# Optimization experiments

Hardware: AMD Instinct MI355X
Metric: run time of the kernel (lower is better)

Reference implementation:

```python
import jax, jax.numpy as jnp
import numpy as np

B, T, V, CI = 1024, 256, 90, 128  # batch, in_channels(=frames), joints(hardcoded 90), inter_channels
EPS = 1e-5


def _bn(x, g, b, m, v):
    # BatchNorm1d in eval mode over channel dim of (B, C, V)
    return (x - m[None, :, None]) * (g * jax.lax.rsqrt(v + EPS))[None, :, None] + b[None, :, None]


def _conv1x1(x, w, b):
    # Conv1d kernel_size=1: (B, Cin, V) x (Cout, Cin) -> (B, Cout, V)
    return jnp.einsum('btv,ct->bcv', x, w) + b[None, :, None]


def setup_inputs() -> dict:
    key = jax.random.key(0)
    ks = iter(jax.random.split(key, 64))
    def nrm(shape, scale=1.0):
        return jax.random.normal(next(ks), shape, jnp.float32) * scale
    p = {}
    p['x1'] = nrm((B, T, V))
    p['x2'] = nrm((B, T, V))
    for nm in ('g', 'th', 'ph'):
        p[nm + '_bn_g'] = 1.0 + 0.1 * nrm((T,))
        p[nm + '_bn_b'] = 0.1 * nrm((T,))
        p[nm + '_bn_m'] = 0.1 * nrm((T,))
        p[nm + '_bn_v'] = jax.random.uniform(next(ks), (T,), jnp.float32, 0.5, 1.5)
        p[nm + '_w'] = nrm((CI, T), T ** -0.5)
        p[nm + '_b'] = 0.01 * nrm((CI,))
    p['W_w'] = nrm((T, CI), CI ** -0.5)
    p['W_b'] = 0.01 * nrm((T,))
    p['W_bn_g'] = 1.0 + 0.1 * nrm((T,))
    p['W_bn_b'] = 0.1 * nrm((T,))
    p['W_bn_m'] = 0.1 * nrm((T,))
    p['W_bn_v'] = jax.random.uniform(next(ks), (T,), jnp.float32, 0.5, 1.5)
    p['qt_w'] = nrm((CI, T), T ** -0.5); p['qt_b'] = 0.01 * nrm((CI,))
    p['ks_w'] = nrm((CI, V), V ** -0.5); p['ks_b'] = 0.01 * nrm((CI,))
    p['qs_w'] = nrm((CI, V), V ** -0.5); p['qs_b'] = 0.01 * nrm((CI,))
    p['kt_w'] = nrm((CI, T), T ** -0.5); p['kt_b'] = 0.01 * nrm((CI,))
    return p


def reference(x1, x2, g_bn_g, g_bn_b, g_bn_m, g_bn_v, g_w, g_b,
              th_bn_g, th_bn_b, th_bn_m, th_bn_v, th_w, th_b,
              ph_bn_g, ph_bn_b, ph_bn_m, ph_bn_v, ph_w, ph_b,
              W_w, W_b, W_bn_g, W_bn_b, W_bn_m, W_bn_v,
              qt_w, qt_b, ks_w, ks_b, qs_w, qs_b, kt_w, kt_b):
    # non-local branch projections (note: phi is applied to x2, theta only to x1)
    g_x1 = _conv1x1(_bn(x1, g_bn_g, g_bn_b, g_bn_m, g_bn_v), g_w, g_b)       # (B,CI,V)
    g_x2 = _conv1x1(_bn(x2, g_bn_g, g_bn_b, g_bn_m, g_bn_v), g_w, g_b)
    theta_x1 = _conv1x1(_bn(x1, th_bn_g, th_bn_b, th_bn_m, th_bn_v), th_w, th_b)
    phi_x1 = _conv1x1(_bn(x2, ph_bn_g, ph_bn_b, ph_bn_m, ph_bn_v), ph_w, ph_b)

    E_t = jnp.einsum('bcv,bdv->bcd', theta_x1, phi_x1)  # (B,CI,CI) = theta_x1 @ phi_x2^T
    E_s = jnp.einsum('bcv,bcw->bvw', theta_x1, phi_x1)  # (B,V,V)  = theta_x2 @ phi_x1
    attn_time_1 = jax.nn.softmax(E_t, axis=-1)
    attn_time_2 = jax.nn.softmax(E_t.transpose(0, 2, 1), axis=-1)
    attn_space_2 = jax.nn.softmax(E_s, axis=-1)            # softmax(energy_space_1)
    attn_space_1 = jax.nn.softmax(E_s.transpose(0, 2, 1), axis=-1)

    z1 = jnp.einsum('bcd,bdv,bvw->bcw', attn_time_2, g_x1, attn_space_2)  # (B,CI,V)
    z2 = jnp.einsum('bcd,bdv,bvw->bcw', attn_time_1, g_x2, attn_space_1)

    # cross interaction (1x1 attention: softmax over singleton dim -> 1, zero grad, kept for faithfulness)
    x1m_v = x1.mean(2)   # (B,T)
    x2m_t = x2.mean(1)   # (B,V)
    x1m_t = x1.mean(1)   # (B,V)
    x2m_v = x2.mean(2)   # (B,T)
    q_time = x1m_v @ qt_w.T + qt_b
    k_space = x2m_t @ ks_w.T + ks_b
    a_t2s = jax.nn.softmax(jnp.sum(q_time * k_space, -1, keepdims=True), axis=-1)[:, 0]  # (B,) == 1
    cross_t2s = a_t2s[:, None, None] * x1m_v[:, :, None]   # (B,T,1)
    q_space = x1m_t @ qs_w.T + qs_b
    k_time = x2m_v @ kt_w.T + kt_b
    a_s2t = jax.nn.softmax(jnp.sum(q_space * k_time, -1, keepdims=True), axis=-1)[:, 0]
    cross_s2t = a_s2t[:, None, None] * x2m_t[:, None, :]   # (B,1,V)

    # W: Conv1d(CI->T,1) then BatchNorm1d(T)
    proj1 = _bn(jnp.einsum('bcv,tc->btv', z1, W_w) + W_b[None, :, None], W_bn_g, W_bn_b, W_bn_m, W_bn_v)
    proj2 = _bn(jnp.einsum('bcv,tc->btv', z2, W_w) + W_b[None, :, None], W_bn_g, W_bn_b, W_bn_m, W_bn_v)

    w1 = jax.nn.softmax(jnp.stack([x1.mean((1, 2)), cross_s2t.mean((1, 2)), proj1.mean((1, 2))], axis=1), axis=1)
    fused_x1 = (w1[:, 0, None, None] * x1 + w1[:, 1, None, None] * cross_s2t
                + w1[:, 2, None, None] * proj1)
    w2 = jax.nn.softmax(jnp.stack([x2.mean((1, 2)), cross_t2s.mean((1, 2)), proj2.mean((1, 2))], axis=1), axis=1)
    fused_x2 = (w2[:, 0, None, None] * x2 + w2[:, 1, None, None] * cross_t2s
                + w2[:, 2, None, None] * proj2)
    return fused_x1, fused_x2
```

## Files before the change

### kernel.cpp

```cpp
#include <hip/hip_runtime.h>

typedef unsigned int u32;
typedef _Float16 f16;
typedef short s16;
typedef _Float16 f16x8 __attribute__((ext_vector_type(8)));
typedef short bf16x8 __attribute__((ext_vector_type(8)));
typedef float f32x4 __attribute__((ext_vector_type(4)));

#define MFMA16(a,b,c) __builtin_amdgcn_mfma_f32_16x16x32_f16(a,b,c,0,0,0)
#define MFMABF(a,b,c) __builtin_amdgcn_mfma_f32_16x16x32_bf16(a,b,c,0,0,0)

namespace {

constexpr int VV = 90, BTV = 256*90, NB = 1024, NT = 1024;

constexpr int XT  = 0;
constexpr int UT  = 0;
constexpr int OS1 = 0;
constexpr int US  = 17408;
constexpr int G1T = 26768;
constexpr int THT = 39824;
constexpr int PHT = 52880;
constexpr int X2  = 52880;
constexpr int G2T = 66448;
constexpr int M1o = 39824;
constexpr int M2o = 53136;
constexpr int Z1o = 26768;
constexpr int Z2o = 66448;
constexpr int OS2 = 39824;
constexpr int SBASE = 79504;
constexpr int oX1MV=0, oX2MT=256, oMRT=352, oISRT=480, oMCT=608, oISCT=736,
              oMRS=864, oISRS=960, oISCS=1056, oSCAL=1152, oMSP=1168;
constexpr int oRED1=608, oRED2=736;
constexpr int SWORDS = 1184;
constexpr int SMEM_BYTES = SBASE*2 + SWORDS*4;

constexpr size_t wThP=0, wGP=65536, wPhP=131072, wWP=196608,
  wBeTh=262144, wBeG=262656, wBePh=263168, wBwe=263680, wCsw=264704, wBwsum=265216;

__device__ __forceinline__ int swz(int row, int col){
  return col ^ (((row >> 3) & 3) << 4);
}

__device__ __forceinline__ f16x8 frag_ld(const f16* p, int stride){
  int l = threadIdx.x & 63;
  return *(const f16x8*)(p + (l & 15) * stride + (l >> 4) * 8);
}
__device__ __forceinline__ bf16x8 bfrag_ld(const s16* p, int stride){
  int l = threadIdx.x & 63;
  return *(const bf16x8*)(p + (l & 15) * stride + (l >> 4) * 8);
}
__device__ __forceinline__ f16x8 frag_ld_sw(const f16* p, int stride, int rowbase, int colbase){
  int l = threadIdx.x & 63;
  int row = rowbase + (l & 15);
  int col = (colbase + (l >> 4) * 8) ^ (((row >> 3) & 3) << 4);
  return *(const f16x8*)(p + row * stride + col);
}
__device__ __forceinline__ bf16x8 bfrag_ld_sw(const s16* p, int stride, int rowbase, int colbase){
  int l = threadIdx.x & 63;
  int row = rowbase + (l & 15);
  int col = (colbase + (l >> 4) * 8) ^ (((row >> 3) & 3) << 4);
  return *(const bf16x8*)(p + row * stride + col);
}
__device__ __forceinline__ s16 f2bf(float x){
  u32 u = __float_as_uint(x);
  u += 0x7FFFu + ((u >> 16) & 1u);
  return (s16)(u >> 16);
}
__device__ __forceinline__ float bf2f(s16 h){
  return __uint_as_float(((u32)(unsigned short)h) << 16);
}

__global__ void prep_weights(
    const float* __restrict__ th_w, const float* __restrict__ th_b,
    const float* __restrict__ th_bng, const float* __restrict__ th_bnb,
    const float* __restrict__ th_bnm, const float* __restrict__ th_bnv,
    const float* __restrict__ g_w, const float* __restrict__ g_b,
    const float* __restrict__ g_bng, const float* __restrict__ g_bnb,
    const float* __restrict__ g_bnm, const float* __restrict__ g_bnv,
    const float* __restrict__ ph_w, const float* __restrict__ ph_b,
    const float* __restrict__ ph_bng, const float* __restrict__ ph_bnb,
    const float* __restrict__ ph_bnm, const float* __restrict__ ph_bnv,
    const float* __restrict__ W_w, const float* __restrict__ W_b,
    const float* __restrict__ W_bng, const float* __restrict__ W_bnb,
    const float* __restrict__ W_bnm, const float* __restrict__ W_bnv,
    char* __restrict__ ws)
{
  __shared__ float red[256];
  const int b = blockIdx.x, tid = threadIdx.x;
  f16* ThP = (f16*)(ws + wThP); f16* GP = (f16*)(ws + wGP);
  f16* PhP = (f16*)(ws + wPhP); s16* WP = (s16*)(ws + wWP);
  float* beTh = (float*)(ws + wBeTh); float* beG = (float*)(ws + wBeG);
  float* bePh = (float*)(ws + wBePh); float* bwe = (float*)(ws + wBwe);
  float* csw = (float*)(ws + wCsw); float* bwsum = (float*)(ws + wBwsum);
  if (b < 128){
    const int c = b, t = tid;
    {
      float s = th_bng[t] * rsqrtf(th_bnv[t] + 1e-5f);
      float d = th_bnb[t] - th_bnm[t] * s;
      float w = th_w[c*256 + t];
      ThP[c*256 + t] = (f16)(w * s);
      red[tid] = w * d; __syncthreads();
      for (int o = 128; o > 0; o >>= 1){ if (tid < o) red[tid] += red[tid+o]; __syncthreads(); }
      if (tid == 0) beTh[c] = th_b[c] + red[0];
      __syncthreads();
    }
    {
      float s = g_bng[t] * rsqrtf(g_bnv[t] + 1e-5f);
      float d = g_bnb[t] - g_bnm[t] * s;
      float w = g_w[c*256 + t];
      GP[c*256 + t] = (f16)(w * s);
      red[tid] = w * d; __syncthreads();
      for (int o = 128; o > 0; o >>= 1){ if (tid < o) red[tid] += red[tid+o]; __syncthreads(); }
      if (tid == 0) beG[c] = g_b[c] + red[0];
      __syncthreads();
    }
    {
      float s = ph_bng[t] * rsqrtf(ph_bnv[t] + 1e-5f);
      float d = ph_bnb[t] - ph_bnm[t] * s;
      float w = ph_w[c*256 + t];
      PhP[c*256 + t] = (f16)(w * s);
      red[tid] = w * d; __syncthreads();
      for (int o = 128; o > 0; o >>= 1){ if (tid < o) red[tid] += red[tid+o]; __syncthreads(); }
      if (tid == 0) bePh[c] = ph_b[c] + red[0];
    }
  } else {
    const int t = (b - 128) * 2 + (tid >> 7);
    const int c = tid & 127;
    float sW = W_bng[t] * rsqrtf(W_bnv[t] + 1e-5f);
    WP[t*128 + c] = f2bf(W_w[t*128 + c] * sW);
    if (c == 0) bwe[t] = (W_b[t] - W_bnm[t]) * sW + W_bnb[t];
    {
      const int c2 = b - 128;
      float sT = W_bng[tid] * rsqrtf(W_bnv[tid] + 1e-5f);
      red[tid] = W_w[tid*128 + c2] * sT;
      __syncthreads();
      for (int o = 128; o > 0; o >>= 1){ if (tid < o) red[tid] += red[tid+o]; __syncthreads(); }
      if (tid == 0) csw[c2] = red[0];
      __syncthreads();
      if (b == 128){
        red[tid] = (W_b[tid] - W_bnm[tid]) * sT + W_bnb[tid];
        __syncthreads();
        for (int o = 128; o > 0; o >>= 1){ if (tid < o) red[tid] += red[tid+o]; __syncthreads(); }
        if (tid == 0) bwsum[0] = red[0];
      }
    }
  }
}

__global__ __launch_bounds__(NT, 1)
void stacif_main(const float* __restrict__ x1g, const float* __restrict__ x2g,
                 const char* __restrict__ ws, float* __restrict__ outg)
{
  extern __shared__ f16 sm[];
  float* Sf = (float*)(sm + SBASE);
  const int tid = threadIdx.x, bid = blockIdx.x;
  const int wid = tid >> 6, l = tid & 63;
  const float* __restrict__ x1b = x1g + (size_t)bid * BTV;
  const float* __restrict__ x2b = x2g + (size_t)bid * BTV;
  const f16* ThP = (const f16*)(ws + wThP);
  const f16* GP  = (const f16*)(ws + wGP);
  const f16* PhP = (const f16*)(ws + wPhP);
  const s16* WP  = (const s16*)(ws + wWP);
  const float* beTh = (const float*)(ws + wBeTh);
  const float* beG  = (const float*)(ws + wBeG);
  const float* bePh = (const float*)(ws + wBePh);
  const float* bwe  = (const float*)(ws + wBwe);
  const float* csw  = (const float*)(ws + wCsw);
  const float* bwsum = (const float*)(ws + wBwsum);
  s16* Up  = (s16*)(sm + UT);
  s16* USp = (s16*)(sm + US);

  const int tS = tid >> 2, qS = tid & 3, vB = qS * 23;

  {
    float r1[23];
    const float* p1 = x1b + tS * 90;
    #pragma unroll
    for (int j = 0; j < 23; ++j){
      int off = vB + j; off = (off < 90) ? off : 89;
      r1[j] = p1[off];
    }
    float a = 0.f;
    #pragma unroll
    for (int j = 0; j < 23; ++j) if (vB + j < 90) a += r1[j];
    a += __shfl_xor(a, 1); a += __shfl_xor(a, 2);
    if (qS == 0) Sf[oX1MV + tS] = a * (1.f/90.f);
    #pragma unroll
    for (int j = 0; j < 23; ++j){
      int v = vB + j;
      if (v < 90) sm[XT + v*272 + tS] = (f16)r1[j];
    }
  }
  {
    float r2[23];
    const float* p2 = x2b + tS * 90;
    #pragma unroll
    for (int j = 0; j < 23; ++j){
      int off = vB + j; off = (off < 90) ? off : 89;
      r2[j] = p2[off];
    }
    #pragma unroll
    for (int j = 0; j < 23; ++j){
      int v = vB + j;
      if (v < 90) sm[X2 + v*272 + tS] = (f16)r2[j];
    }
  }
  __syncthreads();

  {
    const int mat = wid >> 3;
    const int c0 = (wid & 7) * 16;
    const f16* Wm = mat ? GP : ThP;
    const float* beg = mat ? beG : beTh;
    f32x4 acc[6] = {};
    #pragma unroll
    for (int kk = 0; kk < 8; ++kk){
      f16x8 bfr = frag_ld(Wm + c0*256 + kk*32, 256);
      #pragma unroll
      for (int vt = 0; vt < 6; ++vt){
        f16x8 a = frag_ld(sm + XT + vt*16*272 + kk*32, 272);
        acc[vt] = MFMA16(a, bfr, acc[vt]);
      }
    }
    int c = c0 + (l & 15);
    float bias = beg[c];
    #pragma unroll
    for (int vt = 0; vt < 6; ++vt){
      #pragma unroll
      for (int r = 0; r < 4; ++r){
        int v = vt*16 + (l >> 4)*4 + r;
        float val = acc[vt][r] + bias;
        if (mat) ((s16*)(sm + G1T))[v*136 + c] = (v < VV) ? f2bf(val) : (s16)0;
        else     sm[THT + v*136 + swz(v, c)] = (v < VV) ? (f16)val : (f16)0.0f;
      }
    }
  }
  __syncthreads();

  if (tid < 768){
    int v = tid >> 3, p = tid & 7;
    float a = 0.f;
    for (int j = 0; j < 32; ++j) a += (float)sm[X2 + v*272 + p*32 + j];
    a += __shfl_xor(a, 1); a += __shfl_xor(a, 2); a += __shfl_xor(a, 4);
    if (p == 0 && v < VV) Sf[oX2MT + v] = a * (1.f/256.f);
  }
  {
    const int mat = wid >> 3;
    const int c0 = (wid & 7) * 16;
    const f16* Wm = mat ? GP : PhP;
    const float* beg = mat ? beG : bePh;
    f32x4 acc[6] = {};
    #pragma unroll
    for (int kk = 0; kk < 8; ++kk){
      f16x8 bfr = frag_ld(Wm + c0*256 + kk*32, 256);
      #pragma unroll
      for (int vt = 0; vt < 6; ++vt){
        f16x8 a = frag_ld(sm + X2 + vt*16*272 + kk*32, 272);
        acc[vt] = MFMA16(a, bfr, acc[vt]);
      }
    }
    __syncthreads();
    int c = c0 + (l & 15);
    float bias = beg[c];
    #pragma unroll
    for (int vt = 0; vt < 6; ++vt){
      #pragma unroll
      for (int r = 0; r < 4; ++r){
        int v = vt*16 + (l >> 4)*4 + r;
        float val = acc[vt][r] + bias;
        if (mat) ((s16*)(sm + G2T))[v*136 + c] = (v < VV) ? f2bf(val) : (s16)0;
        else     sm[PHT + v*136 + swz(v, c)] = (v < VV) ? (f16)val : (f16)0.0f;
      }
    }
  }
  __syncthreads();

  if (wid < 8){
    int c0 = wid * 16;
    int ca = c0 + (l & 15);
    f32x4 acc[8] = {};
    for (int kk = 0; kk < 3; ++kk){
      int vb = kk*32 + (l >> 4) * 8;
      int cas = swz(vb, ca);
      f16x8 a;
      #pragma unroll
      for (int bb = 0; bb < 8; ++bb) a[bb] = sm[THT + (vb + bb)*136 + cas];
      #pragma unroll
      for (int dt = 0; dt < 8; ++dt){
        int das = swz(vb, dt*16 + (l & 15));
        f16x8 bf;
        #pragma unroll
        for (int bb = 0; bb < 8; ++bb) bf[bb] = sm[PHT + (vb + bb)*136 + das];
        acc[dt] = MFMA16(a, bf, acc[dt]);
      }
    }
    #pragma unroll
    for (int dt = 0; dt < 8; ++dt){
      float m4 = fmaxf(fmaxf(acc[dt][0], acc[dt][1]), fmaxf(acc[dt][2], acc[dt][3]));
      m4 = fmaxf(m4, __shfl_xor(m4, 16));
      m4 = fmaxf(m4, __shfl_xor(m4, 32));
      if (l < 16) Up[(dt*16 + l)*136 + 128 + wid] = f2bf(m4);
    }
    #pragma unroll
    for (int r = 0; r < 4; ++r){
      float m = -3e38f;
      #pragma unroll
      for (int dt = 0; dt < 8; ++dt) m = fmaxf(m, acc[dt][r]);
      for (int sh = 1; sh < 16; sh <<= 1) m = fmaxf(m, __shfl_xor(m, sh));
      float s = 0.f;
      #pragma unroll
      for (int dt = 0; dt < 8; ++dt){ float e = __expf(acc[dt][r] - m); acc[dt][r] = e; s += e; }
      for (int sh = 1; sh < 16; sh <<= 1) s += __shfl_xor(s, sh);
      int row = c0 + (l >> 4)*4 + r;
      if ((l & 15) == 0){ Sf[oMRT + row] = m; Sf[oISRT + row] = 1.f / s; }
      #pragma unroll
      for (int dt = 0; dt < 8; ++dt) Up[row*136 + swz(row, dt*16 + (l & 15))] = f2bf(acc[dt][r]);
    }
  } else if (wid < 14){
    int v0 = (wid - 8) * 16;
    f32x4 acc[6] = {};
    for (int kk = 0; kk < 4; ++kk){
      f16x8 a = frag_ld_sw(sm + THT, 136, v0, kk*32);
      #pragma unroll
      for (int wt = 0; wt < 6; ++wt){
        f16x8 bfr = frag_ld_sw(sm + PHT, 136, wt*16, kk*32);
        acc[wt] = MFMA16(a, bfr, acc[wt]);
      }
    }
    float wmax = -3e38f;
    #pragma unroll
    for (int r = 0; r < 4; ++r){
      float m = 0.f;
      #pragma unroll
      for (int wt = 0; wt < 6; ++wt) m = fmaxf(m, acc[wt][r]);
      for (int sh = 1; sh < 16; sh <<= 1) m = fmaxf(m, __shfl_xor(m, sh));
      float s = 0.f;
      #pragma unroll
      for (int wt = 0; wt < 6; ++wt){
        float e = __expf(acc[wt][r] - m);
        bool valid = (wt*16 + (l & 15)) < VV;
        acc[wt][r] = valid ? e : 0.f;
        s += acc[wt][r];
      }
      for (int sh = 1; sh < 16; sh <<= 1) s += __shfl_xor(s, sh);
      int row = v0 + (l >> 4)*4 + r;
      if ((l & 15) == 0){ Sf[oMRS + row] = m; Sf[oISRS + row] = 1.f / s; }
      if (row < VV) wmax = fmaxf(wmax, m);
      if (row < VV){
        #pragma unroll
        for (int wt = 0; wt < 6; ++wt) USp[row*104 + wt*16 + (l & 15)] = f2bf(acc[wt][r]);
      }
    }
    wmax = fmaxf(wmax, __shfl_xor(wmax, 16));
    wmax = fmaxf(wmax, __shfl_xor(wmax, 32));
    if (l == 0) Sf[oMSP + (wid - 8)] = wmax;
  }
  __syncthreads();

  {
    int ch = wid >> 1;
    int c = (wid & 1) * 64 + l;
    bf16x8 pm8 = *(const bf16x8*)(Up + c*136 + 128);
    float mp = bf2f(pm8[0]);
    #pragma unroll
    for (int q = 1; q < 8; ++q) mp = fmaxf(mp, bf2f(pm8[q]));
    float s = 0.f;
    #pragma unroll
    for (int j = 0; j < 16; ++j){
      int d = ch*16 + j;
      float u = bf2f(Up[d*136 + swz(d, c)]);
      if (u > 0.f){
        float e1 = __expf(0.5f * (Sf[oMRT + d] - mp));
        s += (u * e1) * e1;
      }
    }
    float* PT = (float*)(sm + THT);
    PT[ch*128 + c] = s;
    if (ch == 0) PT[1024 + c] = mp;
  }
  if (tid < 768){
    int v = tid >> 3, p = tid & 7;
    float Ms = Sf[oMSP + 0];
    #pragma unroll
    for (int q = 1; q < 6; ++q) Ms = fmaxf(Ms, Sf[oMSP + q]);
    float s = 0.f;
    for (int j = 0; j < 12; ++j){
      int w = p*12 + j;
      if (w < VV){
        float u = bf2f(USp[w*104 + v]);
        if (u > 0.f) s += u * __expf(Sf[oMRS + w] - Ms);
      }
    }
    s += __shfl_xor(s, 1); s += __shfl_xor(s, 2); s += __shfl_xor(s, 4);
    if (p == 0) Sf[oISCS + v] = 1.f / fmaxf(s, 1e-30f);
  }
  if (tid == 0){
    float Ms = Sf[oMSP + 0];
    #pragma unroll
    for (int q = 1; q < 6; ++q) Ms = fmaxf(Ms, Sf[oMSP + q]);
    Sf[oSCAL + 8] = Ms;
  }
  __syncthreads();
  if (tid < 128){
    const float* PT = (const float*)(sm + THT);
    float s = 0.f;
    #pragma unroll
    for (int q = 0; q < 8; ++q) s += PT[q*128 + tid];
    Sf[oMCT + tid] = PT[1024 + tid];
    Sf[oISCT + tid] = 1.f / s;
  }
  __syncthreads();

  if (wid < 8){
    int c0 = wid * 16;
    const s16* G1 = (const s16*)(sm + G1T);
    s16* M1 = (s16*)(sm + M1o);
    int ca = c0 + (l & 15);
    float mctc = Sf[oMCT + ca];
    f32x4 acc[6] = {};
    #pragma unroll
    for (int kk = 0; kk < 4; ++kk){
      int db = kk*32 + (l >> 4) * 8;
      int cas = swz(db, ca);
      bf16x8 a;
      #pragma unroll
      for (int bb = 0; bb < 8; ++bb){
        float u = bf2f(Up[(db + bb)*136 + cas]);
        float val = 0.f;
        if (u > 0.f){
          float e1 = __expf(0.5f * (Sf[oMRT + db + bb] - mctc));
          val = (u * e1) * e1;
        }
        a[bb] = f2bf(val);
      }
      #pragma unroll
      for (int vt = 0; vt < 6; ++vt){
        bf16x8 bfv = bfrag_ld(G1 + vt*16*136 + kk*32, 136);
        acc[vt] = MFMABF(a, bfv, acc[vt]);
      }
    }
    #pragma unroll
    for (int vt = 0; vt < 6; ++vt){
      int v = vt*16 + (l & 15);
      float cs = (v < VV) ? Sf[oISRS + v] : 0.f;
      #pragma unroll
      for (int r = 0; r < 4; ++r){
        int c = c0 + (l >> 4)*4 + r;
        M1[c*104 + v] = f2bf(acc[vt][r] * Sf[oISCT + c] * cs);
      }
    }
  } else {
    int c0 = (wid - 8) * 16;
    const s16* G2 = (const s16*)(sm + G2T);
    s16* M2 = (s16*)(sm + M2o);
    f32x4 acc[6] = {};
    #pragma unroll
    for (int kk = 0; kk < 4; ++kk){
      bf16x8 a = bfrag_ld_sw(Up, 136, c0, kk*32);
      #pragma unroll
      for (int vt = 0; vt < 6; ++vt){
        bf16x8 bfv = bfrag_ld(G2 + vt*16*136 + kk*32, 136);
        acc[vt] = MFMABF(a, bfv, acc[vt]);
      }
    }
    #pragma unroll
    for (int vt = 0; vt < 6; ++vt){
      int v = vt*16 + (l & 15);
      float cs = (v < VV) ? Sf[oISCS + v] : 0.f;
      #pragma unroll
      for (int r = 0; r < 4; ++r){
        int c = c0 + (l >> 4)*4 + r;
        M2[c*104 + v] = f2bf(acc[vt][r] * Sf[oISRT + c] * cs);
      }
    }
  }
  __syncthreads();

  for (int pass = 0; pass < 3; ++pass){
    int u = wid + pass*16;
    bool isZ2 = u >= 24;
    int rem = isZ2 ? u - 24 : u;
    int w0 = (rem >> 2) * 16;
    int cq = rem & 3;
    int wa = w0 + (l & 15);
    const s16* Mx = (const s16*)(sm + (isZ2 ? M2o : M1o));
    s16* Z = (s16*)(sm + (isZ2 ? Z2o : Z1o));
    int wr = (wa < VV) ? wa : (VV - 1);
    float e_row = isZ2 ? __expf(Sf[oMRS + wr] - Sf[oSCAL + 8]) : 0.f;
    f32x4 acc[2] = {};
    #pragma unroll
    for (int kk = 0; kk < 3; ++kk){
      int vb = kk*32 + (l >> 4) * 8;
      bf16x8 a;
      if (!isZ2){
        #pragma unroll
        for (int bb = 0; bb < 8; ++bb){
          int v = vb + bb;
          a[bb] = (v < VV) ? USp[v*104 + wa] : (s16)0;
        }
      } else {
        bf16x8 uv = *(const bf16x8*)(USp + wr*104 + vb);
        #pragma unroll
        for (int bb = 0; bb < 8; ++bb){
          a[bb] = f2bf(bf2f(uv[bb]) * e_row);
        }
      }
      #pragma unroll
      for (int ct = 0; ct < 2; ++ct){
        bf16x8 bfv = bfrag_ld(Mx + (cq*2 + ct)*16*104 + kk*32, 104);
        acc[ct] = MFMABF(a, bfv, acc[ct]);
      }
    }
    #pragma unroll
    for (int ct = 0; ct < 2; ++ct){
      #pragma unroll
      for (int r = 0; r < 4; ++r){
        int row = w0 + (l >> 4)*4 + r;
        Z[row*136 + (cq*2 + ct)*16 + (l & 15)] = f2bf(acc[ct][r]);
      }
    }
  }
  __syncthreads();

  {
    int col = tid >> 3, zi = (tid >> 2) & 1, p = tid & 3;
    const s16* Z = (const s16*)(sm + (zi ? Z2o : Z1o));
    float s = 0.f;
    for (int j = 0; j < 23; ++j){
      int w = p*23 + j;
      if (w < VV) s += bf2f(Z[w*136 + col]);
    }
    s += __shfl_xor(s, 1); s += __shfl_xor(s, 2);
    if (p == 0){
      float* R = Sf + (zi ? oRED2 : oRED1);
      R[col] = csw[col] * s;
    }
  }
  __syncthreads();
  if (wid == 0){
    float s1 = Sf[oRED1 + l] + Sf[oRED1 + 64 + l];
    float s2 = Sf[oRED2 + l] + Sf[oRED2 + 64 + l];
    float t1 = Sf[oX1MV + l] + Sf[oX1MV + 64 + l] + Sf[oX1MV + 128 + l] + Sf[oX1MV + 192 + l];
    float t2 = (l < VV) ? Sf[oX2MT + l] : 0.f;
    if (l < 26) t2 += Sf[oX2MT + 64 + l];
    for (int sh = 1; sh < 64; sh <<= 1){
      s1 += __shfl_xor(s1, sh);
      s2 += __shfl_xor(s2, sh);
      t1 += __shfl_xor(t1, sh);
      t2 += __shfl_xor(t2, sh);
    }
    if (l == 0){
      float m1 = t1 * (1.f/256.f);
      float m2 = t2 * (1.f/90.f);
      float bws = bwsum[0];
      float mp1 = (s1 + 90.f*bws) * (1.f/23040.f);
      float mp2 = (s2 + 90.f*bws) * (1.f/23040.f);
      {
        float mx = fmaxf(m1, fmaxf(m2, mp1));
        float e0 = __expf(m1-mx), e1 = __expf(m2-mx), e2 = __expf(mp1-mx);
        float inv = 1.f/(e0+e1+e2);
        Sf[oSCAL+0] = e0*inv; Sf[oSCAL+1] = e1*inv; Sf[oSCAL+2] = e2*inv;
      }
      {
        float mx = fmaxf(m2, fmaxf(m1, mp2));
        float e0 = __expf(m2-mx), e1 = __expf(m1-mx), e2 = __expf(mp2-mx);
        float inv = 1.f/(e0+e1+e2);
        Sf[oSCAL+3] = e0*inv; Sf[oSCAL+4] = e1*inv; Sf[oSCAL+5] = e2*inv;
      }
    }
  }
  __syncthreads();

  for (int pass = 0; pass < 2; ++pass){
    int u = wid + pass*16;
    bool is2 = u & 1;
    int t0 = (u >> 1) * 16;
    const s16* Zp = (const s16*)(sm + (is2 ? Z2o : Z1o));
    f32x4 acc[6] = {};
    #pragma unroll
    for (int kk = 0; kk < 4; ++kk){
      bf16x8 a = bfrag_ld(WP + t0*128 + kk*32, 128);
      #pragma unroll
      for (int vt = 0; vt < 6; ++vt){
        bf16x8 bfr = bfrag_ld(Zp + vt*16*136 + kk*32, 136);
        acc[vt] = MFMABF(a, bfr, acc[vt]);
      }
    }
    f16* OS = sm + (is2 ? OS2 : OS1);
    float wb = is2 ? Sf[oSCAL+4] : Sf[oSCAL+1];
    float wc = is2 ? Sf[oSCAL+5] : Sf[oSCAL+2];
    #pragma unroll
    for (int r = 0; r < 4; ++r){
      int t = t0 + (l >> 4)*4 + r;
      float bw = bwe[t];
      float crossv = is2 ? Sf[oX1MV + t] : 0.f;
      #pragma unroll
      for (int vt = 0; vt < 6; ++vt){
        int v = vt*16 + (l & 15);
        if (v < VV){
          float cross = is2 ? crossv : Sf[oX2MT + v];
          OS[t*90 + v] = (f16)(wb * cross + wc * (acc[vt][r] + bw));
        }
      }
    }
  }
  __syncthreads();

  {
    float* out1 = outg + (size_t)bid * BTV;
    float* out2 = outg + (size_t)NB * BTV + (size_t)bid * BTV;
    const float4* x14 = (const float4*)x1b;
    const float4* x24 = (const float4*)x2b;
    float wa1 = Sf[oSCAL+0], wa2 = Sf[oSCAL+3];
    #pragma unroll
    for (int k = 0; k < 3; ++k){
      int e = (k*1024 + tid) * 8;
      if (e < BTV){
        float4 xa = x14[e/4], xb4 = x14[e/4 + 1];
        float4 xc = x24[e/4], xd4 = x24[e/4 + 1];
        f16x8 h1 = *(const f16x8*)(sm + OS1 + e);
        f16x8 h2 = *(const f16x8*)(sm + OS2 + e);
        float4 a1 = {wa1*xa.x + (float)h1[0], wa1*xa.y + (float)h1[1],
                     wa1*xa.z + (float)h1[2], wa1*xa.w + (float)h1[3]};
        float4 b1 = {wa1*xb4.x + (float)h1[4], wa1*xb4.y + (float)h1[5],
                     wa1*xb4.z + (float)h1[6], wa1*xb4.w + (float)h1[7]};
        float4 a2 = {wa2*xc.x + (float)h2[0], wa2*xc.y + (float)h2[1],
                     wa2*xc.z + (float)h2[2], wa2*xc.w + (float)h2[3]};
        float4 b2 = {wa2*xd4.x + (float)h2[4], wa2*xd4.y + (float)h2[5],
                     wa2*xd4.z + (float)h2[6], wa2*xd4.w + (float)h2[7]};
        *(float4*)(out1 + e)     = a1;
        *(float4*)(out1 + e + 4) = b1;
        *(float4*)(out2 + e)     = a2;
        *(float4*)(out2 + e + 4) = b2;
      }
    }
  }
}

}

extern "C" void kernel_launch(void* const* d_in, const int* in_sizes, int n_in,
                              void* d_out, int out_size, void* d_ws, size_t ws_size,
                              hipStream_t stream)
{
  (void)in_sizes; (void)n_in; (void)out_size; (void)ws_size;
  hipFuncSetAttribute((const void*)stacif_main,
                      hipFuncAttributeMaxDynamicSharedMemorySize, SMEM_BYTES);

  const float* x1 = (const float*)d_in[0];
  const float* x2 = (const float*)d_in[1];
  const float* g_bng = (const float*)d_in[2];
  const float* g_bnb = (const float*)d_in[3];
  const float* g_bnm = (const float*)d_in[4];
  const float* g_bnv = (const float*)d_in[5];
  const float* g_w   = (const float*)d_in[6];
  const float* g_b   = (const float*)d_in[7];
  const float* th_bng = (const float*)d_in[8];
  const float* th_bnb = (const float*)d_in[9];
  const float* th_bnm = (const float*)d_in[10];
  const float* th_bnv = (const float*)d_in[11];
  const float* th_w   = (const float*)d_in[12];
  const float* th_b   = (const float*)d_in[13];
  const float* ph_bng = (const float*)d_in[14];
  const float* ph_bnb = (const float*)d_in[15];
  const float* ph_bnm = (const float*)d_in[16];
  const float* ph_bnv = (const float*)d_in[17];
  const float* ph_w   = (const float*)d_in[18];
  const float* ph_b   = (const float*)d_in[19];
  const float* W_w    = (const float*)d_in[20];
  const float* W_b    = (const float*)d_in[21];
  const float* W_bng  = (const float*)d_in[22];
  const float* W_bnb  = (const float*)d_in[23];
  const float* W_bnm  = (const float*)d_in[24];
  const float* W_bnv  = (const float*)d_in[25];
  char* ws = (char*)d_ws;
  float* out = (float*)d_out;

  prep_weights<<<dim3(256), dim3(256), 0, stream>>>(
      th_w, th_b, th_bng, th_bnb, th_bnm, th_bnv,
      g_w, g_b, g_bng, g_bnb, g_bnm, g_bnv,
      ph_w, ph_b, ph_bng, ph_bnb, ph_bnm, ph_bnv,
      W_w, W_b, W_bng, W_bnb, W_bnm, W_bnv, ws);
  stacif_main<<<dim3(NB), dim3(NT), SMEM_BYTES, stream>>>(x1, x2, ws, out);
}
```

Before: 240.7 us.

## Store transposed theta/phi copies in LDS for vector MFMA fragment loads

The theta and phi projections are now written twice to shared memory: row-major without the XOR swizzle, and also transposed (channel-major, stride 104) into the region the x tile used before. The channel-attention GEMM then loads contiguous 8-wide fragments instead of gathering eight scalar f16 values per fragment, and the spatial GEMM drops its swizzled loads. Extra barriers are added so the transposed copies do not overwrite the input tile while it is still being read, and both GEMMs finish before their softmax writes. This trades extra LDS stores, possible bank conflicts from removing the swizzle, and an added barrier for much cheaper fragment loads.

```diff
diff --git a/kernel.cpp b/kernel.cpp
--- a/kernel.cpp
+++ b/kernel.cpp
@@ -15,6 +15,8 @@
 constexpr int VV = 90, BTV = 256*90, NB = 1024, NT = 1024;
 
 constexpr int XT  = 0;
+constexpr int TH2 = 0;
+constexpr int PH2 = 13312;
 constexpr int UT  = 0;
 constexpr int OS1 = 0;
 constexpr int US  = 17408;
@@ -49,12 +51,6 @@
 __device__ __forceinline__ bf16x8 bfrag_ld(const s16* p, int stride){
   int l = threadIdx.x & 63;
   return *(const bf16x8*)(p + (l & 15) * stride + (l >> 4) * 8);
-}
-__device__ __forceinline__ f16x8 frag_ld_sw(const f16* p, int stride, int rowbase, int colbase){
-  int l = threadIdx.x & 63;
-  int row = rowbase + (l & 15);
-  int col = (colbase + (l >> 4) * 8) ^ (((row >> 3) & 3) << 4);
-  return *(const f16x8*)(p + row * stride + col);
 }
 __device__ __forceinline__ bf16x8 bfrag_ld_sw(const s16* p, int stride, int rowbase, int colbase){
   int l = threadIdx.x & 63;
@@ -223,6 +219,7 @@
         acc[vt] = MFMA16(a, bfr, acc[vt]);
       }
     }
+    __syncthreads();
     int c = c0 + (l & 15);
     float bias = beg[c];
     #pragma unroll
@@ -231,8 +228,13 @@
       for (int r = 0; r < 4; ++r){
         int v = vt*16 + (l >> 4)*4 + r;
         float val = acc[vt][r] + bias;
-        if (mat) ((s16*)(sm + G1T))[v*136 + c] = (v < VV) ? f2bf(val) : (s16)0;
-        else     sm[THT + v*136 + swz(v, c)] = (v < VV) ? (f16)val : (f16)0.0f;
+        if (mat){
+          ((s16*)(sm + G1T))[v*136 + c] = (v < VV) ? f2bf(val) : (s16)0;
+        } else {
+          f16 h = (v < VV) ? (f16)val : (f16)0.0f;
+          sm[THT + v*136 + c] = h;
+          sm[TH2 + c*104 + v] = h;
+        }
       }
     }
   }
@@ -269,92 +271,98 @@
       for (int r = 0; r < 4; ++r){
         int v = vt*16 + (l >> 4)*4 + r;
         float val = acc[vt][r] + bias;
-        if (mat) ((s16*)(sm + G2T))[v*136 + c] = (v < VV) ? f2bf(val) : (s16)0;
-        else     sm[PHT + v*136 + swz(v, c)] = (v < VV) ? (f16)val : (f16)0.0f;
-      }
-    }
-  }
-  __syncthreads();
-
-  if (wid < 8){
-    int c0 = wid * 16;
-    int ca = c0 + (l & 15);
+        if (mat){
+          ((s16*)(sm + G2T))[v*136 + c] = (v < VV) ? f2bf(val) : (s16)0;
+        } else {
+          f16 h = (v < VV) ? (f16)val : (f16)0.0f;
+          sm[PHT + v*136 + c] = h;
+          sm[PH2 + c*104 + v] = h;
+        }
+      }
+    }
+  }
+  __syncthreads();
+
+  {
     f32x4 acc[8] = {};
-    for (int kk = 0; kk < 3; ++kk){
-      int vb = kk*32 + (l >> 4) * 8;
-      int cas = swz(vb, ca);
-      f16x8 a;
-      #pragma unroll
-      for (int bb = 0; bb < 8; ++bb) a[bb] = sm[THT + (vb + bb)*136 + cas];
+    if (wid < 8){
+      int c0 = wid * 16;
+      #pragma unroll
+      for (int kk = 0; kk < 3; ++kk){
+        f16x8 a = frag_ld(sm + TH2 + c0*104 + kk*32, 104);
+        #pragma unroll
+        for (int dt = 0; dt < 8; ++dt){
+          f16x8 bfr = frag_ld(sm + PH2 + dt*16*104 + kk*32, 104);
+          acc[dt] = MFMA16(a, bfr, acc[dt]);
+        }
+      }
+    } else if (wid < 14){
+      int v0 = (wid - 8) * 16;
+      #pragma unroll
+      for (int kk = 0; kk < 4; ++kk){
+        f16x8 a = frag_ld(sm + THT + v0*136 + kk*32, 136);
+        #pragma unroll
+        for (int wt = 0; wt < 6; ++wt){
+          f16x8 bfr = frag_ld(sm + PHT + wt*16*136 + kk*32, 136);
+          acc[wt] = MFMA16(a, bfr, acc[wt]);
+        }
+      }
+    }
+    __syncthreads();
+    if (wid < 8){
+      int c0 = wid * 16;
       #pragma unroll
       for (int dt = 0; dt < 8; ++dt){
-        int das = swz(vb, dt*16 + (l & 15));
-        f16x8 bf;
-        #pragma unroll
-        for (int bb = 0; bb < 8; ++bb) bf[bb] = sm[PHT + (vb + bb)*136 + das];
-        acc[dt] = MFMA16(a, bf, acc[dt]);
-      }
-    }
-    #pragma unroll
-    for (int dt = 0; dt < 8; ++dt){
-      float m4 = fmaxf(fmaxf(acc[dt][0], acc[dt][1]), fmaxf(acc[dt][2], acc[dt][3]));
-      m4 = fmaxf(m4, __shfl_xor(m4, 16));
-      m4 = fmaxf(m4, __shfl_xor(m4, 32));
-      if (l < 16) Up[(dt*16 + l)*136 + 128 + wid] = f2bf(m4);
-    }
-    #pragma unroll
-    for (int r = 0; r < 4; ++r){
-      float m = -3e38f;
-      #pragma unroll
-      for (int dt = 0; dt < 8; ++dt) m = fmaxf(m, acc[dt][r]);
-      for (int sh = 1; sh < 16; sh <<= 1) m = fmaxf(m, __shfl_xor(m, sh));
-      float s = 0.f;
-      #pragma unroll
-      for (int dt = 0; dt < 8; ++dt){ float e = __expf(acc[dt][r] - m); acc[dt][r] = e; s += e; }
-      for (int sh = 1; sh < 16; sh <<= 1) s += __shfl_xor(s, sh);
-      int row = c0 + (l >> 4)*4 + r;
-      if ((l & 15) == 0){ Sf[oMRT + row] = m; Sf[oISRT + row] = 1.f / s; }
-      #pragma unroll
-      for (int dt = 0; dt < 8; ++dt) Up[row*136 + swz(row, dt*16 + (l & 15))] = f2bf(acc[dt][r]);
-    }
-  } else if (wid < 14){
-    int v0 = (wid - 8) * 16;
-    f32x4 acc[6] = {};
-    for (int kk = 0; kk < 4; ++kk){
-      f16x8 a = frag_ld_sw(sm + THT, 136, v0, kk*32);
-      #pragma unroll
-      for (int wt = 0; wt < 6; ++wt){
-        f16x8 bfr = frag_ld_sw(sm + PHT, 136, wt*16, kk*32);
-        acc[wt] = MFMA16(a, bfr, acc[wt]);
-      }
-    }
-    float wmax = -3e38f;
-    #pragma unroll
-    for (int r = 0; r < 4; ++r){
-      float m = 0.f;
-      #pragma unroll
-      for (int wt = 0; wt < 6; ++wt) m = fmaxf(m, acc[wt][r]);
-      for (int sh = 1; sh < 16; sh <<= 1) m = fmaxf(m, __shfl_xor(m, sh));
-      float s = 0.f;
-      #pragma unroll
-      for (int wt = 0; wt < 6; ++wt){
-        float e = __expf(acc[wt][r] - m);
-        bool valid = (wt*16 + (l & 15)) < VV;
-        acc[wt][r] = valid ? e : 0.f;
-        s += acc[wt][r];
-      }
-      for (int sh = 1; sh < 16; sh <<= 1) s += __shfl_xor(s, sh);
-      int row = v0 + (l >> 4)*4 + r;
-      if ((l & 15) == 0){ Sf[oMRS + row] = m; Sf[oISRS + row] = 1.f / s; }
-      if (row < VV) wmax = fmaxf(wmax, m);
-      if (row < VV){
-        #pragma unroll
-        for (int wt = 0; wt < 6; ++wt) USp[row*104 + wt*16 + (l & 15)] = f2bf(acc[wt][r]);
-      }
-    }
-    wmax = fmaxf(wmax, __shfl_xor(wmax, 16));
-    wmax = fmaxf(wmax, __shfl_xor(wmax, 32));
-    if (l == 0) Sf[oMSP + (wid - 8)] = wmax;
+        float m4 = fmaxf(fmaxf(acc[dt][0], acc[dt][1]), fmaxf(acc[dt][2], acc[dt][3]));
+        m4 = fmaxf(m4, __shfl_xor(m4, 16));
+        m4 = fmaxf(m4, __shfl_xor(m4, 32));
+        if (l < 16) Up[(dt*16 + l)*136 + 128 + wid] = f2bf(m4);
+      }
+      #pragma unroll
+      for (int r = 0; r < 4; ++r){
+        float m = -3e38f;
+        #pragma unroll
+        for (int dt = 0; dt < 8; ++dt) m = fmaxf(m, acc[dt][r]);
+        for (int sh = 1; sh < 16; sh <<= 1) m = fmaxf(m, __shfl_xor(m, sh));
+        float s = 0.f;
+        #pragma unroll
+        for (int dt = 0; dt < 8; ++dt){ float e = __expf(acc[dt][r] - m); acc[dt][r] = e; s += e; }
+        for (int sh = 1; sh < 16; sh <<= 1) s += __shfl_xor(s, sh);
+        int row = c0 + (l >> 4)*4 + r;
+        if ((l & 15) == 0){ Sf[oMRT + row] = m; Sf[oISRT + row] = 1.f / s; }
+        #pragma unroll
+        for (int dt = 0; dt < 8; ++dt) Up[row*136 + swz(row, dt*16 + (l & 15))] = f2bf(acc[dt][r]);
+      }
+    } else if (wid < 14){
+      int v0 = (wid - 8) * 16;
+      float wmax = -3e38f;
+      #pragma unroll
+      for (int r = 0; r < 4; ++r){
+        float m = 0.f;
+        #pragma unroll
+        for (int wt = 0; wt < 6; ++wt) m = fmaxf(m, acc[wt][r]);
+        for (int sh = 1; sh < 16; sh <<= 1) m = fmaxf(m, __shfl_xor(m, sh));
+        float s = 0.f;
+        #pragma unroll
+        for (int wt = 0; wt < 6; ++wt){
+          float e = __expf(acc[wt][r] - m);
+          bool valid = (wt*16 + (l & 15)) < VV;
+          acc[wt][r] = valid ? e : 0.f;
+          s += acc[wt][r];
+        }
+        for (int sh = 1; sh < 16; sh <<= 1) s += __shfl_xor(s, sh);
+        int row = v0 + (l >> 4)*4 + r;
+        if ((l & 15) == 0){ Sf[oMRS + row] = m; Sf[oISRS + row] = 1.f / s; }
+        if (row < VV) wmax = fmaxf(wmax, m);
+        if (row < VV){
+          #pragma unroll
+          for (int wt = 0; wt < 6; ++wt) USp[row*104 + wt*16 + (l & 15)] = f2bf(acc[wt][r]);
+        }
+      }
+      wmax = fmaxf(wmax, __shfl_xor(wmax, 16));
+      wmax = fmaxf(wmax, __shfl_xor(wmax, 32));
+      if (l == 0) Sf[oMSP + (wid - 8)] = wmax;
+    }
   }
   __syncthreads();
 
```

New measurement: 236.7 us. Within noise of the previous version (-1.7%).
